# Optimization experiments

Hardware: AMD Instinct MI355X
Metric: run time of the kernel (lower is better)

The kernel has to match this reference:

```python
import jax, jax.numpy as jnp
import numpy as np

N_USER, N_MOVIE, E, H, L = 100000, 20000, 1000000, 64, 2
NEG_SLOPE = 0.2  # PyG GATv2Conv default negative_slope


def _rand_edges(k, n_src, n_dst, e):
    k1, k2 = jax.random.split(k)
    src = jax.random.randint(k1, (e,), 0, n_src, dtype=jnp.int32)
    dst = jax.random.randint(k2, (e,), 0, n_dst, dtype=jnp.int32)
    # ensure no src==dst index collisions so PyG's remove_self_loops is a no-op
    dst = jnp.where(dst == src, (dst + 1) % n_dst, dst)
    return jnp.stack([src, dst])


def setup_inputs() -> dict:
    key = jax.random.key(0)
    ks = jax.random.split(key, 8)
    return {
        "x_user": jax.random.normal(ks[0], (N_USER, H), jnp.float32),
        "x_movie": jax.random.normal(ks[1], (N_MOVIE, H), jnp.float32),
        "edge_u2m": _rand_edges(ks[2], N_USER, N_MOVIE, E),
        "edge_m2u": _rand_edges(ks[3], N_MOVIE, N_USER, E),
        # params stacked as [layer, edge_type, ...]; edge_type 0 = user->movie, 1 = movie->user
        "Wl": jax.random.normal(ks[4], (L, 2, H, H), jnp.float32) / np.sqrt(H).astype(np.float32),
        "bl": jnp.zeros((L, 2, H), jnp.float32),
        "Wr": jax.random.normal(ks[5], (L, 2, H, H), jnp.float32) / np.sqrt(H).astype(np.float32),
        "br": jnp.zeros((L, 2, H), jnp.float32),
        "att": jax.random.normal(ks[6], (L, 2, H), jnp.float32) / np.sqrt(H).astype(np.float32),
        "bias": jnp.zeros((L, 2, H), jnp.float32),
    }


def _segment_softmax(scores, seg, n):
    # numerically-stable softmax over variable-degree dst neighborhoods (PyG softmax)
    m = jax.ops.segment_max(scores, seg, num_segments=n)
    ex = jnp.exp(scores - m[seg])
    s = jax.ops.segment_sum(ex, seg, num_segments=n)
    return ex / (s[seg] + 1e-16)


def _gatv2(x_src, x_dst, edge, Wl, bl, Wr, br, att, bias):
    n_src, n_dst = x_src.shape[0], x_dst.shape[0]
    xl = x_src @ Wl + bl  # [N_src, H]
    xr = x_dst @ Wr + br  # [N_dst, H]
    n_loop = min(n_src, n_dst)  # PyG adds self loops with num_nodes = min(N_src, N_dst)
    loop = jnp.arange(n_loop, dtype=edge.dtype)
    src = jnp.concatenate([edge[0], loop])
    dst = jnp.concatenate([edge[1], loop])
    e = jax.nn.leaky_relu(xl[src] + xr[dst], NEG_SLOPE)  # [E', H] gathered per edge
    score = e @ att  # [E']
    alpha = _segment_softmax(score, dst, n_dst)
    out = jax.ops.segment_sum(xl[src] * alpha[:, None], dst, num_segments=n_dst)
    return out + bias


def reference(x_user, x_movie, edge_u2m, edge_m2u, Wl, bl, Wr, br, att, bias):
    for l in range(L):
        new_movie = _gatv2(x_user, x_movie, edge_u2m,
                           Wl[l, 0], bl[l, 0], Wr[l, 0], br[l, 0], att[l, 0], bias[l, 0])
        new_user = _gatv2(x_movie, x_user, edge_m2u,
                          Wl[l, 1], bl[l, 1], Wr[l, 1], br[l, 1], att[l, 1], bias[l, 1])
        x_movie = jax.nn.selu(new_movie)
        x_user = jax.nn.selu(new_user)
    return x_user, x_movie
```

## Files before the change

### kernel.cpp

```cpp
#include <hip/hip_runtime.h>
#include <hip/hip_fp16.h>
#include <cstdint>

#define H 64
#define EPR 16
#define NB 120

__device__ __forceinline__ float selu_f(float x) {
  const float sc = 1.0507009873554805f;
  const float al = 1.6732632423543772f;
  return x > 0.f ? sc * x : sc * al * (expf(x) - 1.f);
}

__global__ __launch_bounds__(256) void gemm64_split(
    const float* __restrict__ Au, const float* __restrict__ Am,
    const float* __restrict__ W0u, const float* __restrict__ b0u,
    const float* __restrict__ W1u, const float* __restrict__ b1u,
    const float* __restrict__ W0m, const float* __restrict__ b0m,
    const float* __restrict__ W1m, const float* __restrict__ b1m,
    __half* __restrict__ C0u, float* __restrict__ C1u,
    __half* __restrict__ C0m, float* __restrict__ C1m,
    int Nu, int Nm, int su, int sm) {
  __shared__ float Ws[64 * 64];
  __shared__ float As[128][65];
  __shared__ float bs[64];

  const int b = blockIdx.x;
  const float *A, *W, *bias; __half* Ch = nullptr; float* Cf = nullptr;
  int N, blk; bool half_out;
  if (b < su)             { A = Au; W = W0u; bias = b0u; Ch = C0u; N = Nu; blk = b;             half_out = true; }
  else if (b < 2 * su)    { A = Au; W = W1u; bias = b1u; Cf = C1u; N = Nu; blk = b - su;        half_out = false; }
  else if (b < 2*su + sm) { A = Am; W = W0m; bias = b0m; Ch = C0m; N = Nm; blk = b - 2*su;      half_out = true; }
  else                    { A = Am; W = W1m; bias = b1m; Cf = C1m; N = Nm; blk = b - 2*su - sm; half_out = false; }

  const int tid = threadIdx.x;
  for (int i = tid; i < 1024; i += 256) ((float4*)Ws)[i] = ((const float4*)W)[i];
  if (tid < 64) bs[tid] = bias[tid];

  const int row0 = blk * 128;
  for (int i = tid; i < 2048; i += 256) {
    int r = i >> 4, c4 = i & 15;
    int row = row0 + r;
    float4 v = make_float4(0.f, 0.f, 0.f, 0.f);
    if (row < N) v = ((const float4*)(A + (size_t)row * H))[c4];
    As[r][c4 * 4 + 0] = v.x;
    As[r][c4 * 4 + 1] = v.y;
    As[r][c4 * 4 + 2] = v.z;
    As[r][c4 * 4 + 3] = v.w;
  }
  __syncthreads();

  const int g = tid & 3;
  const int tr = tid >> 2;
  float acc0[16], acc1[16];
#pragma unroll
  for (int j = 0; j < 16; ++j) { acc0[j] = bs[g * 16 + j]; acc1[j] = bs[g * 16 + j]; }

  for (int k = 0; k < 64; ++k) {
    float a0 = As[tr][k];
    float a1 = As[tr + 64][k];
    const float4* wr = (const float4*)&Ws[k * 64 + g * 16];
#pragma unroll
    for (int c = 0; c < 4; ++c) {
      float4 w = wr[c];
      acc0[4 * c + 0] = fmaf(a0, w.x, acc0[4 * c + 0]);
      acc0[4 * c + 1] = fmaf(a0, w.y, acc0[4 * c + 1]);
      acc0[4 * c + 2] = fmaf(a0, w.z, acc0[4 * c + 2]);
      acc0[4 * c + 3] = fmaf(a0, w.w, acc0[4 * c + 3]);
      acc1[4 * c + 0] = fmaf(a1, w.x, acc1[4 * c + 0]);
      acc1[4 * c + 1] = fmaf(a1, w.y, acc1[4 * c + 1]);
      acc1[4 * c + 2] = fmaf(a1, w.z, acc1[4 * c + 2]);
      acc1[4 * c + 3] = fmaf(a1, w.w, acc1[4 * c + 3]);
    }
  }

#pragma unroll
  for (int half = 0; half < 2; ++half) {
    const int row = row0 + tr + 64 * half;
    if (row >= N) continue;
    const float* acc = half ? acc1 : acc0;
    if (half_out) {
      unsigned pu[8];
#pragma unroll
      for (int j2 = 0; j2 < 8; ++j2) {
        __half2 t = __floats2half2_rn(acc[2 * j2], acc[2 * j2 + 1]);
        pu[j2] = *(unsigned*)&t;
      }
      uint4* c0 = (uint4*)(Ch + (size_t)row * H + g * 16);
      c0[0] = make_uint4(pu[0], pu[1], pu[2], pu[3]);
      c0[1] = make_uint4(pu[4], pu[5], pu[6], pu[7]);
    } else {
      float4* c1 = (float4*)(Cf + (size_t)row * H + g * 16);
#pragma unroll
      for (int c = 0; c < 4; ++c)
        c1[c] = make_float4(acc[4 * c + 0], acc[4 * c + 1], acc[4 * c + 2], acc[4 * c + 3]);
    }
  }
}

__global__ __launch_bounds__(256) void bucket_hist(
    const int* __restrict__ ed1, int E1r, int n1e, int sh1, int B1, int* __restrict__ mat1,
    const int* __restrict__ ed2, int E2r, int n2e, int sh2, int B2, int* __restrict__ mat2) {
  __shared__ int hist[640];
  int b = blockIdx.x;
  const int* ed; int Er, ne, sh, Bn, blk; int* mat;
  if (b < NB) { ed = ed1; Er = E1r; ne = n1e; sh = sh1; Bn = B1; mat = mat1; blk = b; }
  else { ed = ed2; Er = E2r; ne = n2e; sh = sh2; Bn = B2; mat = mat2; blk = b - NB; }
  for (int i = threadIdx.x; i < Bn; i += 256) hist[i] = 0;
  __syncthreads();
  int chunk = (ne + NB - 1) / NB;
  int lo = blk * chunk, hi = lo + chunk;
  if (hi > ne) hi = ne;
  for (int e = lo + threadIdx.x; e < hi; e += 256) {
    int d = (e < Er) ? ed[e] : (e - Er);
    atomicAdd(&hist[d >> sh], 1);
  }
  __syncthreads();
  for (int i = threadIdx.x; i < Bn; i += 256) mat[(size_t)i * NB + blk] = hist[i];
}

__global__ __launch_bounds__(256) void scan_partial2(
    const int* __restrict__ cnt1, int n1, int* __restrict__ psum1, int* __restrict__ bsum1,
    const int* __restrict__ cnt2, int n2, int* __restrict__ psum2, int* __restrict__ bsum2,
    int split) {
  __shared__ int sh[256];
  int b = blockIdx.x;
  const int* cnt; int n; int* psum; int* bsum; int lb;
  if (b < split) { cnt = cnt1; n = n1; psum = psum1; bsum = bsum1; lb = b; }
  else { cnt = cnt2; n = n2; psum = psum2; bsum = bsum2; lb = b - split; }
  int i = lb * 256 + threadIdx.x;
  int tid = threadIdx.x;
  sh[tid] = (i < n) ? cnt[i] : 0;
  __syncthreads();
  for (int off = 1; off < 256; off <<= 1) {
    int t = (tid >= off) ? sh[tid - off] : 0;
    __syncthreads();
    if (tid >= off) sh[tid] += t;
    __syncthreads();
  }
  if (i < n) psum[i] = sh[tid];
  if (tid == 255) bsum[lb] = sh[255];
}

__global__ __launch_bounds__(256) void scan_bsums2(
    int* __restrict__ bsum1, int nb1, int* __restrict__ bsum2, int nb2) {
  __shared__ int sh[256];
  const int tid = threadIdx.x;
  for (int which = 0; which < 2; ++which) {
    int* bsum = which ? bsum2 : bsum1;
    int nb = which ? nb2 : nb1;
    int run = 0;
    for (int start = 0; start < nb; start += 256) {
      int i = start + tid;
      int v = (i < nb) ? bsum[i] : 0;
      __syncthreads();
      sh[tid] = v;
      __syncthreads();
      for (int off = 1; off < 256; off <<= 1) {
        int t = (tid >= off) ? sh[tid - off] : 0;
        __syncthreads();
        if (tid >= off) sh[tid] += t;
        __syncthreads();
      }
      if (i < nb) bsum[i] = run + sh[tid] - v;
      run += sh[255];
      __syncthreads();
    }
  }
}

__global__ __launch_bounds__(256) void finalize_excl2(
    const int* __restrict__ cnt1, const int* __restrict__ psum1,
    const int* __restrict__ bsum1, int n1, int* __restrict__ excl1,
    const int* __restrict__ cnt2, const int* __restrict__ psum2,
    const int* __restrict__ bsum2, int n2, int* __restrict__ excl2, int split) {
  int b = blockIdx.x;
  const int *cnt, *psum, *bsum; int n; int* excl; int lb;
  if (b < split) { cnt = cnt1; psum = psum1; bsum = bsum1; n = n1; excl = excl1; lb = b; }
  else { cnt = cnt2; psum = psum2; bsum = bsum2; n = n2; excl = excl2; lb = b - split; }
  int i = lb * 256 + threadIdx.x;
  if (i >= n) return;
  excl[i] = psum[i] + bsum[lb] - cnt[i];
}

__global__ __launch_bounds__(256) void bucket_part(
    const int* __restrict__ es1, const int* __restrict__ ed1, int E1r, int n1e,
    int sh1, int B1, const int* __restrict__ excl1, unsigned* __restrict__ part1,
    const int* __restrict__ es2, const int* __restrict__ ed2, int E2r, int n2e,
    int sh2, int B2, const int* __restrict__ excl2, unsigned* __restrict__ part2) {
  __shared__ int cur[640];
  int b = blockIdx.x;
  const int *es, *ed, *excl; int Er, ne, sh, Bn, blk; unsigned* part;
  if (b < NB) { es = es1; ed = ed1; Er = E1r; ne = n1e; sh = sh1; Bn = B1; excl = excl1; part = part1; blk = b; }
  else { es = es2; ed = ed2; Er = E2r; ne = n2e; sh = sh2; Bn = B2; excl = excl2; part = part2; blk = b - NB; }
  for (int i = threadIdx.x; i < Bn; i += 256) cur[i] = excl[(size_t)i * NB + blk];
  __syncthreads();
  int chunk = (ne + NB - 1) / NB;
  int lo = blk * chunk, hi = lo + chunk;
  if (hi > ne) hi = ne;
  const unsigned lmask = (1u << sh) - 1u;
  for (int e = lo + threadIdx.x; e < hi; e += 256) {
    int s, d;
    if (e < Er) { s = es[e]; d = ed[e]; } else { s = e - Er; d = s; }
    int bkt = d >> sh;
    int pos = atomicAdd(&cur[bkt], 1);
    part[pos] = (((unsigned)d & lmask) << 18) | (unsigned)s;
  }
}

__global__ __launch_bounds__(256) void bucket_sort(
    const unsigned* __restrict__ part1, const int* __restrict__ excl1,
    int n1e, int sh1, int B1, int nd1, int* __restrict__ rp1, int* __restrict__ csr1,
    const unsigned* __restrict__ part2, const int* __restrict__ excl2,
    int n2e, int sh2, int B2, int nd2, int* __restrict__ rp2, int* __restrict__ csr2) {
  __shared__ int cnt_s[256];
  __shared__ int scan_s[256];
  int b = blockIdx.x;
  const unsigned* part; const int* excl; int ne, sh, Bn, nd, bkt; int *rp, *csr;
  if (b < B1) { part = part1; excl = excl1; ne = n1e; sh = sh1; Bn = B1; nd = nd1; rp = rp1; csr = csr1; bkt = b; }
  else { part = part2; excl = excl2; ne = n2e; sh = sh2; Bn = B2; nd = nd2; rp = rp2; csr = csr2; bkt = b - B1; }
  const int tid = threadIdx.x;
  const int dbase = bkt << sh;
  const int R = 1 << sh;
  int rcap = nd - dbase;
  if (rcap > R) rcap = R;
  const int base = excl[(size_t)bkt * NB];
  const int endv = (bkt == Bn - 1) ? ne : excl[(size_t)(bkt + 1) * NB];

  cnt_s[tid] = 0;
  __syncthreads();
  for (int i = base + tid; i < endv; i += 256)
    atomicAdd(&cnt_s[part[i] >> 18], 1);
  __syncthreads();
  int c = cnt_s[tid];
  scan_s[tid] = c;
  __syncthreads();
  for (int off = 1; off < 256; off <<= 1) {
    int t = (tid >= off) ? scan_s[tid - off] : 0;
    __syncthreads();
    if (tid >= off) scan_s[tid] += t;
    __syncthreads();
  }
  if (tid < rcap) rp[dbase + tid + 1] = base + scan_s[tid];
  cnt_s[tid] = base + scan_s[tid] - c;
  if (tid == 0 && bkt == 0) rp[0] = 0;
  __syncthreads();
  for (int i = base + tid; i < endv; i += 256) {
    unsigned p = part[i];
    int dl = p >> 18;
    int pos = atomicAdd(&cnt_s[dl], 1);
    csr[pos] = (int)(p & 0x3FFFFu);
  }
}

__global__ __launch_bounds__(256) void gat_dst2(
    const int* __restrict__ rp1, const int* __restrict__ csr1,
    const __half* __restrict__ xl1, const float* __restrict__ xr1,
    const float* __restrict__ att1, const float* __restrict__ bias1,
    float* __restrict__ out1, int nd1,
    const int* __restrict__ rp2, const int* __restrict__ csr2,
    const __half* __restrict__ xl2, const float* __restrict__ xr2,
    const float* __restrict__ att2, const float* __restrict__ bias2,
    float* __restrict__ out2, int nd2, int split) {
  __shared__ __align__(16) float tile[4][EPR * 64];

  const int b = blockIdx.x;
  const int* rp; const int* csr; const __half* xl; const float *xr, *att, *bias;
  float* out; int nd, d0;
  if (b < split) {
    rp = rp1; csr = csr1; xl = xl1; xr = xr1; att = att1; bias = bias1;
    out = out1; nd = nd1; d0 = b * 4;
  } else {
    rp = rp2; csr = csr2; xl = xl2; xr = xr2; att = att2; bias = bias2;
    out = out2; nd = nd2; d0 = (b - split) * 4;
  }
  const int w = threadIdx.x >> 6;
  const int d = d0 + w;
  if (d >= nd) return;
  const int h = threadIdx.x & 63;
  const unsigned h2 = (unsigned)h * 2u;
  const char* xlb = (const char*)xl;
  float* tl = tile[w];

  const float xr_h = xr[(size_t)d * H + h];
  const float a = att[h];
  const float a06 = 0.6f * a, a04 = 0.4f * a;
  const float bias_h = bias[h];
  const int sbeg = __builtin_amdgcn_readfirstlane(rp[d]);
  const int send = __builtin_amdgcn_readfirstlane(rp[d + 1]);

  const int r = h & 15;
  const int q = h >> 4;
  const int pr = (q << 2) ^ r;

  float o;

  if (send - sbeg <= EPR) {
    const int cnt = send - sbeg;
    const int* csw = csr + sbeg;
    float v[EPR];
#pragma unroll
    for (int qq = 0; qq < EPR / 4; ++qq) {
      if (qq * 4 < cnt) {
#pragma unroll
        for (int i = 0; i < 4; ++i) {
          const int k = qq * 4 + i;
          int j = k < cnt ? k : cnt - 1;
          unsigned src = (unsigned)csw[j];
          v[k] = __half2float(*(const __half*)(xlb + ((src << 7) | h2)));
        }
      }
    }
#pragma unroll
    for (int qq = 0; qq < EPR / 4; ++qq) {
      if (qq * 4 < cnt) {
#pragma unroll
        for (int i = 0; i < 4; ++i) {
          const int k = qq * 4 + i;
          float p = v[k] + xr_h;
          tl[(k << 6) | (h ^ (k << 2))] = fmaf(p, a06, fabsf(p) * a04);
        }
      }
    }
    const float4* t4 = (const float4*)tl;
    float t0 = 0.f, t1 = 0.f, t2 = 0.f, t3 = 0.f;
#pragma unroll
    for (int c = 0; c < 4; ++c) {
      float4 q4 = t4[(r << 4) | (pr ^ c)];
      t0 += q4.x; t1 += q4.y; t2 += q4.z; t3 += q4.w;
    }
    float t = (t0 + t1) + (t2 + t3);
    t += __shfl_xor(t, 16, 64);
    t += __shfl_xor(t, 32, 64);
    t = (r < cnt) ? t : -3.0e38f;

    float M = t;
#pragma unroll
    for (int mk = 1; mk <= 8; mk <<= 1) M = fmaxf(M, __shfl_xor(M, mk, 64));
    float e = __expf(t - M);
    float S = e;
#pragma unroll
    for (int mk = 1; mk <= 8; mk <<= 1) S += __shfl_xor(S, mk, 64);
    if (h < 16) tl[h] = e;

    float P = 0.f;
#pragma unroll
    for (int qq = 0; qq < EPR / 4; ++qq) {
      if (qq * 4 < cnt) {
        float4 w4 = ((const float4*)tl)[qq];
        P += w4.x * v[qq * 4 + 0];
        P += w4.y * v[qq * 4 + 1];
        P += w4.z * v[qq * 4 + 2];
        P += w4.w * v[qq * 4 + 3];
      }
    }
    o = P / (S + 1e-16f) + bias_h;
  } else {
    float m = -3.0e38f, s = 0.f, acc = 0.f;
    int base = sbeg;
    float v[EPR], v2[EPR];

    {
      const int* csw = csr + base;
#pragma unroll
      for (int k = 0; k < EPR; ++k) {
        unsigned src = (unsigned)csw[k];
        v[k] = __half2float(*(const __half*)(xlb + ((src << 7) | h2)));
      }
    }

    auto round = [&](float (&vc)[EPR], float (&vp)[EPR]) -> bool {
      int cnt = send - base;
      if (cnt > EPR) cnt = EPR;
#pragma unroll
      for (int qq = 0; qq < EPR / 4; ++qq) {
        if (qq * 4 < cnt) {
#pragma unroll
          for (int i = 0; i < 4; ++i) {
            const int k = qq * 4 + i;
            float p = vc[k] + xr_h;
            tl[(k << 6) | (h ^ (k << 2))] = fmaf(p, a06, fabsf(p) * a04);
          }
        }
      }
      const int nbase = base + EPR;
      int ncnt = send - nbase;
      const bool have_next = ncnt > 0;
      if (ncnt > EPR) ncnt = EPR;
      if (have_next) {
        const int* csn = csr + nbase;
#pragma unroll
        for (int qq = 0; qq < EPR / 4; ++qq) {
          if (qq * 4 < ncnt) {
#pragma unroll
            for (int i = 0; i < 4; ++i) {
              const int k = qq * 4 + i;
              int j = k < ncnt ? k : ncnt - 1;
              unsigned src = (unsigned)csn[j];
              vp[k] = __half2float(*(const __half*)(xlb + ((src << 7) | h2)));
            }
          }
        }
      }
      const float4* t4 = (const float4*)tl;
      float t0 = 0.f, t1 = 0.f, t2 = 0.f, t3 = 0.f;
#pragma unroll
      for (int c = 0; c < 4; ++c) {
        float4 q4 = t4[(r << 4) | (pr ^ c)];
        t0 += q4.x; t1 += q4.y; t2 += q4.z; t3 += q4.w;
      }
      float t = (t0 + t1) + (t2 + t3);
      t += __shfl_xor(t, 16, 64);
      t += __shfl_xor(t, 32, 64);
      t = (r < cnt) ? t : -3.0e38f;

      float M = t;
#pragma unroll
      for (int mk = 1; mk <= 8; mk <<= 1) M = fmaxf(M, __shfl_xor(M, mk, 64));
      float e = __expf(t - M);
      float S = e;
#pragma unroll
      for (int mk = 1; mk <= 8; mk <<= 1) S += __shfl_xor(S, mk, 64);
      if (h < 16) tl[h] = e;

      float nm = fmaxf(m, M);
      float a_old = __expf(m - nm);
      float a_new = __expf(M - nm);
      float P = 0.f;
#pragma unroll
      for (int qq = 0; qq < EPR / 4; ++qq) {
        if (qq * 4 < cnt) {
          float4 w4 = ((const float4*)tl)[qq];
          P += w4.x * vc[qq * 4 + 0];
          P += w4.y * vc[qq * 4 + 1];
          P += w4.z * vc[qq * 4 + 2];
          P += w4.w * vc[qq * 4 + 3];
        }
      }
      s = s * a_old + S * a_new;
      acc = acc * a_old + P * a_new;
      m = nm;
      base = nbase;
      return have_next;
    };

    for (;;) {
      if (!round(v, v2)) break;
      if (!round(v2, v)) break;
    }
    o = acc / (s + 1e-16f) + bias_h;
  }

  out[(size_t)d * H + h] = selu_f(o);
}

extern "C" void kernel_launch(void* const* d_in, const int* in_sizes, int n_in,
                              void* d_out, int out_size, void* d_ws, size_t ws_size,
                              hipStream_t stream) {
  const float* x_user = (const float*)d_in[0];
  const float* x_movie = (const float*)d_in[1];
  const int* e_u2m = (const int*)d_in[2];
  const int* e_m2u = (const int*)d_in[3];
  const float* Wl = (const float*)d_in[4];
  const float* bl = (const float*)d_in[5];
  const float* Wr = (const float*)d_in[6];
  const float* br = (const float*)d_in[7];
  const float* att = (const float*)d_in[8];
  const float* bias = (const float*)d_in[9];

  const int n_user = in_sizes[0] / H;
  const int n_movie = in_sizes[1] / H;
  const int E1 = in_sizes[2] / 2;
  const int E2 = in_sizes[3] / 2;
  const int n_loop = n_user < n_movie ? n_user : n_movie;
  const int nE1 = E1 + n_loop;
  const int nE2 = E2 + n_loop;

  const int SHM = 5, SHU = 8;
  const int Bm = (n_movie + (1 << SHM) - 1) >> SHM;
  const int Bu = (n_user + (1 << SHU) - 1) >> SHU;
  const int nmatM = Bm * NB, nmatU = Bu * NB;
  const int nbm = (nmatM + 255) / 256, nbu = (nmatU + 255) / 256;

  float* ws = (float*)d_ws;
  size_t o = 0;
  __half* xl_u2m = (__half*)(ws + o); o += (size_t)n_user * H / 2;
  __half* xl_m2u = (__half*)(ws + o); o += (size_t)n_movie * H / 2;
  float* xr_u2m = ws + o; o += (size_t)n_movie * H;
  float* xr_m2u = ws + o; o += (size_t)n_user * H;

  int* matM  = (int*)(ws + o); o += nmatM;
  int* psumM = (int*)(ws + o); o += nmatM;
  int* exclM = (int*)(ws + o); o += nmatM;
  int* matU  = (int*)(ws + o); o += nmatU;
  int* psumU = (int*)(ws + o); o += nmatU;
  int* exclU = (int*)(ws + o); o += nmatU;
  int* bsumM = (int*)(ws + o); o += 1024;
  int* bsumU = (int*)(ws + o); o += 1024;
  unsigned* partM = (unsigned*)(ws + o); o += nE1;
  unsigned* partU = (unsigned*)(ws + o); o += nE2;
  int* csr1 = (int*)(ws + o); o += nE1;
  int* csr2 = (int*)(ws + o); o += nE2;
  int* rp1  = (int*)(ws + o); o += n_movie + 1;
  int* rp2  = (int*)(ws + o); o += n_user + 1;

  float* out_u = (float*)d_out;
  float* out_m = out_u + (size_t)n_user * H;

  const int su = (n_user + 127) / 128;
  const int sm = (n_movie + 127) / 128;
  const int split1 = (n_movie + 3) / 4;
  const int split2 = (n_user + 3) / 4;

  bucket_hist<<<2 * NB, 256, 0, stream>>>(
      e_u2m + E1, E1, nE1, SHM, Bm, matM,
      e_m2u + E2, E2, nE2, SHU, Bu, matU);
  scan_partial2<<<nbm + nbu, 256, 0, stream>>>(
      matM, nmatM, psumM, bsumM, matU, nmatU, psumU, bsumU, nbm);
  scan_bsums2<<<1, 256, 0, stream>>>(bsumM, nbm, bsumU, nbu);
  finalize_excl2<<<nbm + nbu, 256, 0, stream>>>(
      matM, psumM, bsumM, nmatM, exclM,
      matU, psumU, bsumU, nmatU, exclU, nbm);
  bucket_part<<<2 * NB, 256, 0, stream>>>(
      e_u2m, e_u2m + E1, E1, nE1, SHM, Bm, exclM, partM,
      e_m2u, e_m2u + E2, E2, nE2, SHU, Bu, exclU, partU);
  bucket_sort<<<Bm + Bu, 256, 0, stream>>>(
      partM, exclM, nE1, SHM, Bm, n_movie, rp1, csr1,
      partU, exclU, nE2, SHU, Bu, n_user, rp2, csr2);

  for (int l = 0; l < 2; ++l) {
    const float* cu = (l == 0) ? x_user : out_u;
    const float* cm = (l == 0) ? x_movie : out_m;
    const int p0 = l * 2 + 0;
    const int p1 = l * 2 + 1;

    gemm64_split<<<2 * (su + sm), 256, 0, stream>>>(
        cu, cm,
        Wl + (size_t)p0 * H * H, bl + (size_t)p0 * H,
        Wr + (size_t)p1 * H * H, br + (size_t)p1 * H,
        Wl + (size_t)p1 * H * H, bl + (size_t)p1 * H,
        Wr + (size_t)p0 * H * H, br + (size_t)p0 * H,
        xl_u2m, xr_m2u, xl_m2u, xr_u2m,
        n_user, n_movie, su, sm);

    gat_dst2<<<split1 + split2, 256, 0, stream>>>(
        rp1, csr1, xl_u2m, xr_u2m, att + (size_t)p0 * H, bias + (size_t)p0 * H,
        out_m, n_movie,
        rp2, csr2, xl_m2u, xr_m2u, att + (size_t)p1 * H, bias + (size_t)p1 * H,
        out_u, n_user, split1);
  }
}
```

Baseline: 428.0 us.

## Replace bucket-sort CSR build with single cooperative kernel using global atomics

Six kernels (histogram, scans, partition, per-bucket sort) are replaced by one cooperative-launch kernel that counts in-degrees with global atomics, scans them, and scatters edge sources into CSR positions via per-destination atomic cursors, separated by grid syncs. This removes launch overhead and intermediate partition buffers. In exchange it uses global atomics with random destinations, and the scatter order within a row is no longer deterministic.

```diff
diff --git a/kernel.cpp b/kernel.cpp
--- a/kernel.cpp
+++ b/kernel.cpp
@@ -1,10 +1,13 @@
 #include <hip/hip_runtime.h>
+#include <hip/hip_cooperative_groups.h>
 #include <hip/hip_fp16.h>
 #include <cstdint>
 
+namespace cg = cooperative_groups;
+
 #define H 64
 #define EPR 16
-#define NB 120
+#define CSRB 960
 
 __device__ __forceinline__ float selu_f(float x) {
   const float sc = 1.0507009873554805f;
@@ -98,61 +101,55 @@
   }
 }
 
-__global__ __launch_bounds__(256) void bucket_hist(
-    const int* __restrict__ ed1, int E1r, int n1e, int sh1, int B1, int* __restrict__ mat1,
-    const int* __restrict__ ed2, int E2r, int n2e, int sh2, int B2, int* __restrict__ mat2) {
-  __shared__ int hist[640];
-  int b = blockIdx.x;
-  const int* ed; int Er, ne, sh, Bn, blk; int* mat;
-  if (b < NB) { ed = ed1; Er = E1r; ne = n1e; sh = sh1; Bn = B1; mat = mat1; blk = b; }
-  else { ed = ed2; Er = E2r; ne = n2e; sh = sh2; Bn = B2; mat = mat2; blk = b - NB; }
-  for (int i = threadIdx.x; i < Bn; i += 256) hist[i] = 0;
-  __syncthreads();
-  int chunk = (ne + NB - 1) / NB;
-  int lo = blk * chunk, hi = lo + chunk;
-  if (hi > ne) hi = ne;
-  for (int e = lo + threadIdx.x; e < hi; e += 256) {
-    int d = (e < Er) ? ed[e] : (e - Er);
-    atomicAdd(&hist[d >> sh], 1);
-  }
-  __syncthreads();
-  for (int i = threadIdx.x; i < Bn; i += 256) mat[(size_t)i * NB + blk] = hist[i];
-}
-
-__global__ __launch_bounds__(256) void scan_partial2(
-    const int* __restrict__ cnt1, int n1, int* __restrict__ psum1, int* __restrict__ bsum1,
-    const int* __restrict__ cnt2, int n2, int* __restrict__ psum2, int* __restrict__ bsum2,
-    int split) {
-  __shared__ int sh[256];
-  int b = blockIdx.x;
-  const int* cnt; int n; int* psum; int* bsum; int lb;
-  if (b < split) { cnt = cnt1; n = n1; psum = psum1; bsum = bsum1; lb = b; }
-  else { cnt = cnt2; n = n2; psum = psum2; bsum = bsum2; lb = b - split; }
-  int i = lb * 256 + threadIdx.x;
-  int tid = threadIdx.x;
-  sh[tid] = (i < n) ? cnt[i] : 0;
-  __syncthreads();
-  for (int off = 1; off < 256; off <<= 1) {
-    int t = (tid >= off) ? sh[tid - off] : 0;
-    __syncthreads();
-    if (tid >= off) sh[tid] += t;
-    __syncthreads();
-  }
-  if (i < n) psum[i] = sh[tid];
-  if (tid == 255) bsum[lb] = sh[255];
-}
-
-__global__ __launch_bounds__(256) void scan_bsums2(
-    int* __restrict__ bsum1, int nb1, int* __restrict__ bsum2, int nb2) {
+__global__ __launch_bounds__(256) void csr_build(
+    const int* __restrict__ es1, const int* __restrict__ ed1,
+    int E1, int nE1, int nd1, int* cnt1, int* rp1, int* csr1,
+    const int* __restrict__ es2, const int* __restrict__ ed2,
+    int E2, int nE2, int nd2, int* cnt2, int* rp2, int* csr2,
+    int* csum, int C1, int C2) {
+  cg::grid_group grid = cg::this_grid();
   __shared__ int sh[256];
   const int tid = threadIdx.x;
-  for (int which = 0; which < 2; ++which) {
-    int* bsum = which ? bsum2 : bsum1;
-    int nb = which ? nb2 : nb1;
+  const int gsz = gridDim.x;
+  const int gid = blockIdx.x * 256 + tid;
+  const int gstride = gsz * 256;
+
+  for (int e = gid; e < nE1; e += gstride) {
+    int d = (e < E1) ? ed1[e] : (e - E1);
+    atomicAdd(&cnt1[d], 1);
+  }
+  for (int e = gid; e < nE2; e += gstride) {
+    int d = (e < E2) ? ed2[e] : (e - E2);
+    atomicAdd(&cnt2[d], 1);
+  }
+  grid.sync();
+
+  for (int c = blockIdx.x; c < C1 + C2; c += gsz) {
+    const int* cnt; int* rp; int n; int lc;
+    if (c < C1) { cnt = cnt1; rp = rp1; n = nd1; lc = c; }
+    else        { cnt = cnt2; rp = rp2; n = nd2; lc = c - C1; }
+    int i = lc * 256 + tid;
+    int v = (i < n) ? cnt[i] : 0;
+    __syncthreads();
+    sh[tid] = v;
+    __syncthreads();
+    for (int off = 1; off < 256; off <<= 1) {
+      int t = (tid >= off) ? sh[tid - off] : 0;
+      __syncthreads();
+      if (tid >= off) sh[tid] += t;
+      __syncthreads();
+    }
+    if (i < n) rp[i + 1] = sh[tid];
+    if (tid == 255) csum[c] = sh[255];
+    __syncthreads();
+  }
+  grid.sync();
+
+  if (blockIdx.x == 0) {
     int run = 0;
-    for (int start = 0; start < nb; start += 256) {
-      int i = start + tid;
-      int v = (i < nb) ? bsum[i] : 0;
+    for (int start = 0; start < C1; start += 256) {
+      int li = start + tid;
+      int v = (li < C1) ? csum[li] : 0;
       __syncthreads();
       sh[tid] = v;
       __syncthreads();
@@ -162,94 +159,56 @@
         if (tid >= off) sh[tid] += t;
         __syncthreads();
       }
-      if (i < nb) bsum[i] = run + sh[tid] - v;
+      if (li < C1) csum[li] = run + sh[tid] - v;
       run += sh[255];
       __syncthreads();
     }
-  }
-}
-
-__global__ __launch_bounds__(256) void finalize_excl2(
-    const int* __restrict__ cnt1, const int* __restrict__ psum1,
-    const int* __restrict__ bsum1, int n1, int* __restrict__ excl1,
-    const int* __restrict__ cnt2, const int* __restrict__ psum2,
-    const int* __restrict__ bsum2, int n2, int* __restrict__ excl2, int split) {
-  int b = blockIdx.x;
-  const int *cnt, *psum, *bsum; int n; int* excl; int lb;
-  if (b < split) { cnt = cnt1; psum = psum1; bsum = bsum1; n = n1; excl = excl1; lb = b; }
-  else { cnt = cnt2; psum = psum2; bsum = bsum2; n = n2; excl = excl2; lb = b - split; }
-  int i = lb * 256 + threadIdx.x;
-  if (i >= n) return;
-  excl[i] = psum[i] + bsum[lb] - cnt[i];
-}
-
-__global__ __launch_bounds__(256) void bucket_part(
-    const int* __restrict__ es1, const int* __restrict__ ed1, int E1r, int n1e,
-    int sh1, int B1, const int* __restrict__ excl1, unsigned* __restrict__ part1,
-    const int* __restrict__ es2, const int* __restrict__ ed2, int E2r, int n2e,
-    int sh2, int B2, const int* __restrict__ excl2, unsigned* __restrict__ part2) {
-  __shared__ int cur[640];
-  int b = blockIdx.x;
-  const int *es, *ed, *excl; int Er, ne, sh, Bn, blk; unsigned* part;
-  if (b < NB) { es = es1; ed = ed1; Er = E1r; ne = n1e; sh = sh1; Bn = B1; excl = excl1; part = part1; blk = b; }
-  else { es = es2; ed = ed2; Er = E2r; ne = n2e; sh = sh2; Bn = B2; excl = excl2; part = part2; blk = b - NB; }
-  for (int i = threadIdx.x; i < Bn; i += 256) cur[i] = excl[(size_t)i * NB + blk];
-  __syncthreads();
-  int chunk = (ne + NB - 1) / NB;
-  int lo = blk * chunk, hi = lo + chunk;
-  if (hi > ne) hi = ne;
-  const unsigned lmask = (1u << sh) - 1u;
-  for (int e = lo + threadIdx.x; e < hi; e += 256) {
+    run = 0;
+    for (int start = 0; start < C2; start += 256) {
+      int li = start + tid;
+      int v = (li < C2) ? csum[C1 + li] : 0;
+      __syncthreads();
+      sh[tid] = v;
+      __syncthreads();
+      for (int off = 1; off < 256; off <<= 1) {
+        int t = (tid >= off) ? sh[tid - off] : 0;
+        __syncthreads();
+        if (tid >= off) sh[tid] += t;
+        __syncthreads();
+      }
+      if (li < C2) csum[C1 + li] = run + sh[tid] - v;
+      run += sh[255];
+      __syncthreads();
+    }
+  }
+  grid.sync();
+
+  for (int c = blockIdx.x; c < C1 + C2; c += gsz) {
+    int* cnt; int* rp; int n; int lc;
+    if (c < C1) { cnt = cnt1; rp = rp1; n = nd1; lc = c; }
+    else        { cnt = cnt2; rp = rp2; n = nd2; lc = c - C1; }
+    int i = lc * 256 + tid;
+    int off = csum[c];
+    if (i < n) {
+      int incl = rp[i + 1] + off;
+      rp[i + 1] = incl;
+      cnt[i] = incl - cnt[i];
+      if (i == 0) rp[0] = 0;
+    }
+  }
+  grid.sync();
+
+  for (int e = gid; e < nE1; e += gstride) {
     int s, d;
-    if (e < Er) { s = es[e]; d = ed[e]; } else { s = e - Er; d = s; }
-    int bkt = d >> sh;
-    int pos = atomicAdd(&cur[bkt], 1);
-    part[pos] = (((unsigned)d & lmask) << 18) | (unsigned)s;
-  }
-}
-
-__global__ __launch_bounds__(256) void bucket_sort(
-    const unsigned* __restrict__ part1, const int* __restrict__ excl1,
-    int n1e, int sh1, int B1, int nd1, int* __restrict__ rp1, int* __restrict__ csr1,
-    const unsigned* __restrict__ part2, const int* __restrict__ excl2,
-    int n2e, int sh2, int B2, int nd2, int* __restrict__ rp2, int* __restrict__ csr2) {
-  __shared__ int cnt_s[256];
-  __shared__ int scan_s[256];
-  int b = blockIdx.x;
-  const unsigned* part; const int* excl; int ne, sh, Bn, nd, bkt; int *rp, *csr;
-  if (b < B1) { part = part1; excl = excl1; ne = n1e; sh = sh1; Bn = B1; nd = nd1; rp = rp1; csr = csr1; bkt = b; }
-  else { part = part2; excl = excl2; ne = n2e; sh = sh2; Bn = B2; nd = nd2; rp = rp2; csr = csr2; bkt = b - B1; }
-  const int tid = threadIdx.x;
-  const int dbase = bkt << sh;
-  const int R = 1 << sh;
-  int rcap = nd - dbase;
-  if (rcap > R) rcap = R;
-  const int base = excl[(size_t)bkt * NB];
-  const int endv = (bkt == Bn - 1) ? ne : excl[(size_t)(bkt + 1) * NB];
-
-  cnt_s[tid] = 0;
-  __syncthreads();
-  for (int i = base + tid; i < endv; i += 256)
-    atomicAdd(&cnt_s[part[i] >> 18], 1);
-  __syncthreads();
-  int c = cnt_s[tid];
-  scan_s[tid] = c;
-  __syncthreads();
-  for (int off = 1; off < 256; off <<= 1) {
-    int t = (tid >= off) ? scan_s[tid - off] : 0;
-    __syncthreads();
-    if (tid >= off) scan_s[tid] += t;
-    __syncthreads();
-  }
-  if (tid < rcap) rp[dbase + tid + 1] = base + scan_s[tid];
-  cnt_s[tid] = base + scan_s[tid] - c;
-  if (tid == 0 && bkt == 0) rp[0] = 0;
-  __syncthreads();
-  for (int i = base + tid; i < endv; i += 256) {
-    unsigned p = part[i];
-    int dl = p >> 18;
-    int pos = atomicAdd(&cnt_s[dl], 1);
-    csr[pos] = (int)(p & 0x3FFFFu);
+    if (e < E1) { s = es1[e]; d = ed1[e]; } else { s = e - E1; d = s; }
+    int pos = atomicAdd(&cnt1[d], 1);
+    csr1[pos] = s;
+  }
+  for (int e = gid; e < nE2; e += gstride) {
+    int s, d;
+    if (e < E2) { s = es2[e]; d = ed2[e]; } else { s = e - E2; d = s; }
+    int pos = atomicAdd(&cnt2[d], 1);
+    csr2[pos] = s;
   }
 }
 
@@ -476,12 +435,6 @@
   const int nE1 = E1 + n_loop;
   const int nE2 = E2 + n_loop;
 
-  const int SHM = 5, SHU = 8;
-  const int Bm = (n_movie + (1 << SHM) - 1) >> SHM;
-  const int Bu = (n_user + (1 << SHU) - 1) >> SHU;
-  const int nmatM = Bm * NB, nmatU = Bu * NB;
-  const int nbm = (nmatM + 255) / 256, nbu = (nmatU + 255) / 256;
-
   float* ws = (float*)d_ws;
   size_t o = 0;
   __half* xl_u2m = (__half*)(ws + o); o += (size_t)n_user * H / 2;
@@ -489,20 +442,13 @@
   float* xr_u2m = ws + o; o += (size_t)n_movie * H;
   float* xr_m2u = ws + o; o += (size_t)n_user * H;
 
-  int* matM  = (int*)(ws + o); o += nmatM;
-  int* psumM = (int*)(ws + o); o += nmatM;
-  int* exclM = (int*)(ws + o); o += nmatM;
-  int* matU  = (int*)(ws + o); o += nmatU;
-  int* psumU = (int*)(ws + o); o += nmatU;
-  int* exclU = (int*)(ws + o); o += nmatU;
-  int* bsumM = (int*)(ws + o); o += 1024;
-  int* bsumU = (int*)(ws + o); o += 1024;
-  unsigned* partM = (unsigned*)(ws + o); o += nE1;
-  unsigned* partU = (unsigned*)(ws + o); o += nE2;
+  int* cntM = (int*)(ws + o); o += n_movie;
+  int* cntU = (int*)(ws + o); o += n_user;
+  int* rp1  = (int*)(ws + o); o += n_movie + 1;
+  int* rp2  = (int*)(ws + o); o += n_user + 1;
   int* csr1 = (int*)(ws + o); o += nE1;
   int* csr2 = (int*)(ws + o); o += nE2;
-  int* rp1  = (int*)(ws + o); o += n_movie + 1;
-  int* rp2  = (int*)(ws + o); o += n_user + 1;
+  int* csum = (int*)(ws + o); o += 1024;
 
   float* out_u = (float*)d_out;
   float* out_m = out_u + (size_t)n_user * H;
@@ -511,22 +457,25 @@
   const int sm = (n_movie + 127) / 128;
   const int split1 = (n_movie + 3) / 4;
   const int split2 = (n_user + 3) / 4;
-
-  bucket_hist<<<2 * NB, 256, 0, stream>>>(
-      e_u2m + E1, E1, nE1, SHM, Bm, matM,
-      e_m2u + E2, E2, nE2, SHU, Bu, matU);
-  scan_partial2<<<nbm + nbu, 256, 0, stream>>>(
-      matM, nmatM, psumM, bsumM, matU, nmatU, psumU, bsumU, nbm);
-  scan_bsums2<<<1, 256, 0, stream>>>(bsumM, nbm, bsumU, nbu);
-  finalize_excl2<<<nbm + nbu, 256, 0, stream>>>(
-      matM, psumM, bsumM, nmatM, exclM,
-      matU, psumU, bsumU, nmatU, exclU, nbm);
-  bucket_part<<<2 * NB, 256, 0, stream>>>(
-      e_u2m, e_u2m + E1, E1, nE1, SHM, Bm, exclM, partM,
-      e_m2u, e_m2u + E2, E2, nE2, SHU, Bu, exclU, partU);
-  bucket_sort<<<Bm + Bu, 256, 0, stream>>>(
-      partM, exclM, nE1, SHM, Bm, n_movie, rp1, csr1,
-      partU, exclU, nE2, SHU, Bu, n_user, rp2, csr2);
+  const int C1 = (n_movie + 255) / 256;
+  const int C2 = (n_user + 255) / 256;
+
+  hipMemsetAsync(cntM, 0, (size_t)(n_movie + n_user) * sizeof(int), stream);
+  {
+    const int* es1 = e_u2m;      const int* ed1 = e_u2m + E1;
+    const int* es2 = e_m2u;      const int* ed2 = e_m2u + E2;
+    int E1v = E1, nE1v = nE1, nd1v = n_movie;
+    int E2v = E2, nE2v = nE2, nd2v = n_user;
+    int C1v = C1, C2v = C2;
+    void* args[] = {
+      (void*)&es1, (void*)&ed1, (void*)&E1v, (void*)&nE1v, (void*)&nd1v,
+      (void*)&cntM, (void*)&rp1, (void*)&csr1,
+      (void*)&es2, (void*)&ed2, (void*)&E2v, (void*)&nE2v, (void*)&nd2v,
+      (void*)&cntU, (void*)&rp2, (void*)&csr2,
+      (void*)&csum, (void*)&C1v, (void*)&C2v };
+    hipLaunchCooperativeKernel((const void*)csr_build, dim3(CSRB), dim3(256),
+                               args, 0, stream);
+  }
 
   for (int l = 0; l < 2; ++l) {
     const float* cu = (l == 0) ? x_user : out_u;
```

Result: slower. 1.059 ms (+147.5%).
